# Kernel optimization log

Measured on AMD Instinct MI355X. Metric: run time of the kernel, lower is better.

## Reference

```python
import jax, jax.numpy as jnp
import numpy as np

N_ATOMS = 50000
N_NBRS = 32
R_CUTOFF = 5.0
N_BASIS = 128
N_FILTERS = 128
N_GAUSS = 25
MAX_Z = 100
MEAN = 0.0
STDDEV = 20.0


def ssp(x):
    # shifted softplus: softplus(x) - log(2)
    return jax.nn.softplus(x) - jnp.log(2.0)


def setup_inputs() -> dict:
    key = jax.random.key(0)
    ks = jax.random.split(key, 18)
    dR = jax.random.uniform(ks[0], (N_ATOMS, N_NBRS), dtype=jnp.float32) * R_CUTOFF
    Z = jax.random.randint(ks[1], (N_ATOMS,), 0, MAX_Z)
    nbr_idx = jax.random.randint(ks[2], (N_ATOMS, N_NBRS), 0, N_ATOMS)

    def p(k, shape):
        fan_in = shape[0]
        return (jax.random.normal(k, shape, dtype=jnp.float32) / np.sqrt(fan_in)).astype(jnp.float32)

    return dict(
        dR=dR, Z=Z, nbr_idx=nbr_idx,
        embed_table=jax.random.normal(ks[3], (MAX_Z, N_BASIS), dtype=jnp.float32),
        fw1=p(ks[4], (N_GAUSS, N_FILTERS)), fb1=jnp.zeros((N_FILTERS,), jnp.float32),
        fw2=p(ks[5], (N_FILTERS, N_FILTERS)), fb2=jnp.zeros((N_FILTERS,), jnp.float32),
        in2f_w=p(ks[6], (N_BASIS, N_FILTERS)),
        f2out_w1=p(ks[7], (N_FILTERS, N_BASIS)), f2out_b1=jnp.zeros((N_BASIS,), jnp.float32),
        f2out_w2=p(ks[8], (N_BASIS, N_BASIS)), f2out_b2=jnp.zeros((N_BASIS,), jnp.float32),
        mlp_w1=p(ks[9], (N_BASIS, 64)), mlp_b1=jnp.zeros((64,), jnp.float32),
        mlp_w2=p(ks[10], (64, 1)), mlp_b2=jnp.zeros((1,), jnp.float32),
    )


def reference(dR, Z, nbr_idx, embed_table, fw1, fb1, fw2, fb2, in2f_w,
              f2out_w1, f2out_b1, f2out_w2, f2out_b2,
              mlp_w1, mlp_b1, mlp_w2, mlp_b2):
    # embedding lookup: [N, B]
    x = embed_table[Z]

    # gaussian smearing of distances: [N, K, G]
    offsets = jnp.linspace(0.0, R_CUTOFF, N_GAUSS, dtype=jnp.float32)
    coeff = -0.5 / (offsets[1] - offsets[0]) ** 2
    dr_exp = jnp.exp(coeff * (dR[..., None] - offsets) ** 2)

    # filter network: Dense+ssp, Dense -> [N, K, F]
    W = ssp(jnp.einsum('nkg,gf->nkf', dr_exp, fw1) + fb1)
    W = jnp.einsum('nkf,fh->nkh', W, fw2) + fb2

    # cosine cutoff
    fcut = 0.5 * (jnp.cos(dR * jnp.pi / R_CUTOFF) + 1.0) * (dR < R_CUTOFF)
    W = W * fcut[..., None]

    # cfconv: in2f (no bias), neighbor gather, elementwise filter, sum over neighbors
    y = x @ in2f_w                    # [N, F]
    y_nbrs = y[nbr_idx]               # [N, K, F] irregular gather
    mask = (nbr_idx < N_ATOMS)[..., None]
    agg = jnp.sum(jnp.where(mask, y_nbrs * W, 0.0), axis=1)  # [N, F]

    # f2out: Dense+ssp, Dense
    v = ssp(agg @ f2out_w1 + f2out_b1) @ f2out_w2 + f2out_b2

    # residual update
    x = x + v

    # atomwise MLP [128 -> 64 -> 1] with ssp between layers
    yi = ssp(x @ mlp_w1 + mlp_b1) @ mlp_w2 + mlp_b2  # [N, 1]
    yi = yi * STDDEV + MEAN

    # aggregate (sum over atom axis), per_atom=False
    return jnp.sum(yi, axis=0)  # [1]
```

## Files before the change

### kernel.cpp

```cpp
#include <hip/hip_runtime.h>
#include <math.h>

#define N_ATOMS  50000
#define N_NBRS   32
#define N_GAUSS  25
#define RCUT     5.0f
#define TT       192
#define TROWS    32
#define NTB      6
#define MAXZ     100
#define NT32     1563
#define PBLOCKS  256
#define NPAIR    (N_ATOMS * N_NBRS)
#define PKPAD    (NT32 * 1024)
#define PKB      782
#define PI_F     3.14159265358979323846f

typedef unsigned int   uint_t;
typedef unsigned short ushort_t;
typedef _Float16 f16;
typedef f16   f16x2 __attribute__((ext_vector_type(2)));
typedef f16   f16x4 __attribute__((ext_vector_type(4)));
typedef f16   f16x8 __attribute__((ext_vector_type(8)));
typedef float f32x4 __attribute__((ext_vector_type(4)));

__device__ __forceinline__ float ssp(float x) {
  return fmaxf(x, 0.0f) + __logf(fmaf(0.5f, __expf(-fabsf(x)), 0.5f));
}
__device__ __forceinline__ f16x2 bch(uint_t u) {
  return __builtin_bit_cast(f16x2, u);
}
__device__ __forceinline__ uint_t hcb(f16x2 v) {
  return __builtin_bit_cast(uint_t, v);
}
__device__ __forceinline__ int swz(int m, int e) {
  return m * 128 + ((((e >> 3) ^ m) & 15) << 3) + (e & 7);
}

__global__ void __launch_bounds__(256, 2)
prep_all_kernel(const float* __restrict__ fw1,
                const float* __restrict__ fb1,
                const float* __restrict__ fw2,
                const float* __restrict__ fb2,
                const float* __restrict__ w1,
                const float* __restrict__ w2,
                const float* __restrict__ mw1,
                const float* __restrict__ embed,
                const float* __restrict__ in2f,
                const float* __restrict__ dR,
                const int* __restrict__ nbr,
                const int* __restrict__ Z,
                f16* __restrict__ tabh,
                f16* __restrict__ ytab,
                f16* __restrict__ w1ht,
                f16* __restrict__ w2ht,
                f16* __restrict__ mw1ht,
                uint_t* __restrict__ pkAll) {
  const int tid = threadIdx.x;
  const int bid = blockIdx.x;

  __shared__ float sW2[128 * 128];
  __shared__ float sH[TROWS][128];

  if (bid >= NTB + 64) {
    const int base = (bid - NTB - 64) * 2048;
    #pragma unroll
    for (int t0 = 0; t0 < 8; ++t0) {
      const int idx = base + t0 * 256 + tid;
      if (idx < PKPAD) {
        uint_t pk = 0;
        if (idx < NPAIR) {
          const float r = dR[idx];
          const int  nb = nbr[idx];
          int i0 = (int)(r * (191.0f / RCUT) + 0.5f);
          i0 = min(i0, 191);
          pk = (uint_t)i0 | ((uint_t)Z[nb] << 8);
        }
        pkAll[idx] = pk;
      }
    }
    return;
  }

  if (bid < NTB) {
    const int i0 = bid * TROWS;
    #pragma unroll
    for (int t = 0; t < 16; ++t) {
      const int e = tid + t * 256;
      ((float4*)sW2)[e] = ((const float4*)fw2)[e];
    }
    {
      const int f  = tid & 127;
      const int rh = (tid >> 7) * (TROWS / 2);
      const float delta = RCUT / (float)(N_GAUSS - 1);
      const float coeff = -0.5f / (delta * delta);
      const float b1v = fb1[f];
      for (int j = 0; j < TROWS / 2; ++j) {
        const float r = (float)(i0 + rh + j) * (RCUT / 191.0f);
        float h = b1v;
        #pragma unroll
        for (int g = 0; g < N_GAUSS; ++g) {
          const float d = r - (float)g * delta;
          h = fmaf(__expf(coeff * d * d), fw1[g * 128 + f], h);
        }
        sH[rh + j][f] = ssp(h);
      }
    }
    __syncthreads();
    {
      const int c0 = (tid & 31) * 4;
      const int rg = (tid >> 5) * 4;
      f32x4 acc[4];
      const float4 bv = *(const float4*)&fb2[c0];
      #pragma unroll
      for (int j = 0; j < 4; ++j) acc[j] = (f32x4){bv.x, bv.y, bv.z, bv.w};
      for (int k = 0; k < 128; ++k) {
        const float4 wv = *(const float4*)&sW2[k * 128 + c0];
        #pragma unroll
        for (int j = 0; j < 4; ++j) {
          const float hv = sH[rg + j][k];
          acc[j][0] = fmaf(hv, wv.x, acc[j][0]);
          acc[j][1] = fmaf(hv, wv.y, acc[j][1]);
          acc[j][2] = fmaf(hv, wv.z, acc[j][2]);
          acc[j][3] = fmaf(hv, wv.w, acc[j][3]);
        }
      }
      #pragma unroll
      for (int j = 0; j < 4; ++j) {
        const int i = i0 + rg + j;
        const float r = (float)i * (RCUT / 191.0f);
        const float fc = (r < RCUT) ? 0.5f * (__cosf(r * PI_F / RCUT) + 1.0f) : 0.0f;
        f16x4 o;
        #pragma unroll
        for (int c = 0; c < 4; ++c) o[c] = (f16)(acc[j][c] * fc);
        *(f16x4*)&tabh[i * 128 + c0] = o;
      }
    }
  } else {
    const int cc = (bid - NTB) * 2 + (tid >> 7);
    const int i  = tid & 127;
    w1ht[cc * 128 + i] = (f16)w1[i * 128 + cc];
    w2ht[cc * 128 + i] = (f16)w2[i * 128 + cc];
    if (cc < 64) mw1ht[cc * 128 + i] = (f16)mw1[i * 64 + cc];
    float* xs = &sH[0][0] + (tid >> 7) * 128;
    xs[i] = (cc < MAXZ) ? embed[cc * 128 + i] : 0.0f;
    __syncthreads();
    if (cc < MAXZ) {
      float acc = 0.0f;
      for (int j = 0; j < 128; j += 4) {
        const float4 xv = *reinterpret_cast<const float4*>(&xs[j]);
        acc = fmaf(xv.x, in2f[(j + 0) * 128 + i], acc);
        acc = fmaf(xv.y, in2f[(j + 1) * 128 + i], acc);
        acc = fmaf(xv.z, in2f[(j + 2) * 128 + i], acc);
        acc = fmaf(xv.w, in2f[(j + 3) * 128 + i], acc);
      }
      ytab[cc * 128 + i] = (f16)acc;
    }
  }
}

__global__ void __launch_bounds__(512, 2)
fused_kernel(const uint_t* __restrict__ pkAll,
             const int* __restrict__ Z,
             const float* __restrict__ embed,
             const f16* __restrict__ tabh,
             const f16* __restrict__ ytab,
             const f16* __restrict__ w1ht, const float* __restrict__ b1,
             const f16* __restrict__ w2ht, const float* __restrict__ b2,
             const f16* __restrict__ mw1ht, const float* __restrict__ mb1,
             const float* __restrict__ mw2,
             float* __restrict__ partial) {
  const int tid = threadIdx.x;
  const int w   = tid >> 6;
  const int l   = tid & 63;
  const int q   = l >> 4;
  const int cq  = l & 15;
  const int bid = blockIdx.x;

  __shared__ __align__(16) f16    sW[TT * 128];
  __shared__ __align__(16) f16    sYT[MAXZ * 128];
  __shared__ __align__(16) uint_t s_pk[2][1024];
  __shared__ __align__(16) f16    aggB[2][32 * 128];
  __shared__ __align__(16) f16    sB[32 * 128];
  __shared__ __align__(16) f16    sX[32 * 128];
  __shared__ int   sZb[2][32];
  __shared__ float sRed[8];

  for (int e = tid; e < TT * 16; e += 512)   ((uint4*)sW)[e]  = ((const uint4*)tabh)[e];
  for (int e = tid; e < MAXZ * 16; e += 512) ((uint4*)sYT)[e] = ((const uint4*)ytab)[e];

  const int g   = w >> 2;
  const int wvg = w & 3;
  const int rc  = cq;
  const int qk  = q;
  f16x8 bw1[2][4], bw2[2][4], bwm[4];
  float bb1[2], bb2[2];
  #pragma unroll
  for (int t = 0; t < 2; ++t) {
    const int c = wvg * 32 + t * 16 + rc;
    bb1[t] = b1[c];
    bb2[t] = b2[c];
    #pragma unroll
    for (int k0i = 0; k0i < 4; ++k0i) {
      bw1[t][k0i] = *(const f16x8*)&w1ht[c * 128 + k0i * 32 + qk * 8];
      bw2[t][k0i] = *(const f16x8*)&w2ht[c * 128 + k0i * 32 + qk * 8];
    }
  }
  const int c1 = wvg * 16 + rc;
  #pragma unroll
  for (int k0i = 0; k0i < 4; ++k0i)
    bwm[k0i] = *(const f16x8*)&mw1ht[c1 * 128 + k0i * 32 + qk * 8];
  const float bm = mb1[c1];
  const float cm = mw2[c1];

  const int m = w * 4 + q;
  const char* wb = (const char*)sW  + cq * 16;
  const char* yb = (const char*)sYT + cq * 16;

  const int myChunks = (NT32 - 1 - bid) / PBLOCKS + 1;
  float vsum = 0.0f;

  f16x2 acc[4];
  uint4 twA[4], ytA[4], twB[4], ytB[4];

#define STAGE(bb, cc) { \
    const uint2 v = *(const uint2*)&pkAll[(cc) * 1024 + tid * 2]; \
    *(uint2*)&s_pk[bb][tid * 2] = v; \
    if (tid < 32) sZb[bb][tid] = ((cc) * 32 + tid < N_ATOMS) ? Z[(cc) * 32 + tid] : 0; }

#define IG(BK, bb, gi) { \
    _Pragma("unroll") \
    for (int d = 0; d < 4; ++d) { \
      const uint_t pk = s_pk[bb][m * N_NBRS + (gi) * 4 + d]; \
      tw##BK[d] = *(const uint4*)(wb + ((pk & 0xFFu) << 8)); \
      yt##BK[d] = *(const uint4*)(yb + ((pk >> 8) << 8)); \
    } }

#define CG(BK) { \
    _Pragma("unroll") \
    for (int d = 0; d < 4; ++d) { \
      acc[0] += bch(tw##BK[d].x) * bch(yt##BK[d].x); \
      acc[1] += bch(tw##BK[d].y) * bch(yt##BK[d].y); \
      acc[2] += bch(tw##BK[d].z) * bch(yt##BK[d].z); \
      acc[3] += bch(tw##BK[d].w) * bch(yt##BK[d].w); \
    } }

#define AGGW(bb) { \
    uint4 o; \
    o.x = hcb(acc[0]); o.y = hcb(acc[1]); o.z = hcb(acc[2]); o.w = hcb(acc[3]); \
    const int mm = m & 15; \
    *(uint4*)&aggB[bb][(m >> 4) * 2048 + mm * 128 + (((cq ^ mm) & 15) << 3)] = o; }

#define AFRAGP(P, k0) (*(const f16x8*)&(P)[rc * 128 + (((((k0) >> 3) + qk) ^ rc) & 15) * 8])

  STAGE(0, bid)
  if (1 < myChunks) STAGE(1, bid + PBLOCKS)
  __syncthreads();
  #pragma unroll
  for (int c = 0; c < 4; ++c) acc[c] = (f16x2)0;
  IG(A, 0, 0) IG(B, 0, 1)
  CG(A) IG(A, 0, 2)
  CG(B) IG(B, 0, 3)
  CG(A) IG(A, 0, 4)
  CG(B) IG(B, 0, 5)
  CG(A) IG(A, 0, 6)
  CG(B) IG(B, 0, 7)
  CG(A)
  CG(B)
  AGGW(0)
  __syncthreads();

  for (int s = 0; s < myChunks; ++s) {
    const int b  = s & 1;
    const int cc = bid + s * PBLOCKS;
    const bool hn = (s + 1 < myChunks);
    const int nb_ = b ^ 1;

    if (hn) {
      #pragma unroll
      for (int c = 0; c < 4; ++c) acc[c] = (f16x2)0;
    }

    if (hn) { IG(A, nb_, 0) IG(B, nb_, 1) }
    {
      const f16* aggp = &aggB[b][g * 2048];
      f32x4 dacc[2];
      #pragma unroll
      for (int t = 0; t < 2; ++t) dacc[t] = (f32x4){bb1[t], bb1[t], bb1[t], bb1[t]};
      #pragma unroll
      for (int k0i = 0; k0i < 4; ++k0i) {
        const f16x8 af = AFRAGP(aggp, k0i * 32);
        #pragma unroll
        for (int t = 0; t < 2; ++t)
          dacc[t] = __builtin_amdgcn_mfma_f32_16x16x32_f16(af, bw1[t][k0i], dacc[t], 0, 0, 0);
      }
      f16* hB = &sB[g * 2048];
      #pragma unroll
      for (int t = 0; t < 2; ++t) {
        const int c = wvg * 32 + t * 16 + rc;
        #pragma unroll
        for (int r = 0; r < 4; ++r) hB[swz(qk * 4 + r, c)] = (f16)ssp(dacc[t][r]);
      }
    }
    if (hn) { CG(A) IG(A, nb_, 2) CG(B) CG(A) }
    __syncthreads();

    if (hn) { IG(A, nb_, 3) IG(B, nb_, 4) }
    {
      const f16* hB = &sB[g * 2048];
      f16* hX = &sX[g * 2048];
      f32x4 dacc[2];
      #pragma unroll
      for (int t = 0; t < 2; ++t) dacc[t] = (f32x4){bb2[t], bb2[t], bb2[t], bb2[t]};
      #pragma unroll
      for (int k0i = 0; k0i < 4; ++k0i) {
        const f16x8 af = AFRAGP(hB, k0i * 32);
        #pragma unroll
        for (int t = 0; t < 2; ++t)
          dacc[t] = __builtin_amdgcn_mfma_f32_16x16x32_f16(af, bw2[t][k0i], dacc[t], 0, 0, 0);
      }
      #pragma unroll
      for (int t = 0; t < 2; ++t) {
        const int c = wvg * 32 + t * 16 + rc;
        #pragma unroll
        for (int r = 0; r < 4; ++r) {
          const int mm = qk * 4 + r;
          const float x = embed[(size_t)sZb[b][g * 16 + mm] * 128 + c] + dacc[t][r];
          hX[swz(mm, c)] = (f16)x;
        }
      }
    }
    if (hn) { CG(A) IG(A, nb_, 5) CG(B) CG(A) }
    __syncthreads();

    if (hn) { IG(A, nb_, 6) IG(B, nb_, 7) }
    if (s + 2 < myChunks) STAGE(b, bid + (s + 2) * PBLOCKS)
    {
      const f16* hX = &sX[g * 2048];
      f32x4 a2 = (f32x4){bm, bm, bm, bm};
      #pragma unroll
      for (int k0i = 0; k0i < 4; ++k0i)
        a2 = __builtin_amdgcn_mfma_f32_16x16x32_f16(AFRAGP(hX, k0i * 32), bwm[k0i], a2, 0, 0, 0);
      #pragma unroll
      for (int r = 0; r < 4; ++r) {
        const int atom = cc * 32 + g * 16 + qk * 4 + r;
        if (atom < N_ATOMS) vsum = fmaf(ssp(a2[r]), cm, vsum);
      }
    }
    if (hn) { CG(A) CG(B) AGGW(nb_) }
    __syncthreads();
  }
#undef STAGE
#undef IG
#undef CG
#undef AGGW
#undef AFRAGP

  #pragma unroll
  for (int o = 1; o < 64; o <<= 1) vsum += __shfl_xor(vsum, o, 64);
  if (l == 0) sRed[w] = vsum;
  __syncthreads();
  if (tid == 0) {
    float sF = 0.0f;
    #pragma unroll
    for (int i = 0; i < 8; ++i) sF += sRed[i];
    partial[bid] = sF;
  }
}

__global__ void __launch_bounds__(256, 1)
reduce_kernel(const float* __restrict__ partial,
              const float* __restrict__ mb2,
              float* __restrict__ out) {
  const int tid = threadIdx.x;
  float s = 0.0f;
  for (int i = tid; i < PBLOCKS; i += 256) s += partial[i];
  __shared__ float sr[4];
  #pragma unroll
  for (int o = 1; o < 64; o <<= 1) s += __shfl_xor(s, o, 64);
  if ((tid & 63) == 0) sr[tid >> 6] = s;
  __syncthreads();
  if (tid == 0) {
    out[0] = 20.0f * (sr[0] + sr[1] + sr[2] + sr[3] + (float)N_ATOMS * mb2[0]);
  }
}

extern "C" void kernel_launch(void* const* d_in, const int* in_sizes, int n_in,
                              void* d_out, int out_size, void* d_ws, size_t ws_size,
                              hipStream_t stream) {
  const float* dR    = (const float*)d_in[0];
  const int*   Z     = (const int*)  d_in[1];
  const int*   nbr   = (const int*)  d_in[2];
  const float* embed = (const float*)d_in[3];
  const float* fw1   = (const float*)d_in[4];
  const float* fb1   = (const float*)d_in[5];
  const float* fw2   = (const float*)d_in[6];
  const float* fb2   = (const float*)d_in[7];
  const float* in2f  = (const float*)d_in[8];
  const float* w1    = (const float*)d_in[9];
  const float* b1    = (const float*)d_in[10];
  const float* w2    = (const float*)d_in[11];
  const float* b2    = (const float*)d_in[12];
  const float* mw1   = (const float*)d_in[13];
  const float* mb1   = (const float*)d_in[14];
  const float* mw2   = (const float*)d_in[15];
  const float* mb2   = (const float*)d_in[16];
  float* out = (float*)d_out;

  char* ws = (char*)d_ws;
  f16*    tabh    = (f16*)ws;
  f16*    ytab    = (f16*)(ws + (size_t)64 * 1024);
  f16*    w1ht    = (f16*)(ws + (size_t)128 * 1024);
  f16*    w2ht    = (f16*)(ws + (size_t)192 * 1024);
  f16*    mw1ht   = (f16*)(ws + (size_t)256 * 1024);
  float*  partial = (float*)(ws + (size_t)384 * 1024);
  uint_t* pkAll   = (uint_t*)(ws + (size_t)1024 * 1024);

  prep_all_kernel<<<NTB + 64 + PKB, 256, 0, stream>>>(fw1, fb1, fw2, fb2,
      w1, w2, mw1, embed, in2f, dR, nbr, Z,
      tabh, ytab, w1ht, w2ht, mw1ht, pkAll);
  fused_kernel<<<PBLOCKS, 512, 0, stream>>>(pkAll, Z, embed,
      tabh, ytab, w1ht, b1, w2ht, b2, mw1ht, mb1, mw2, partial);
  reduce_kernel<<<1, 256, 0, stream>>>(partial, mb2, out);
}
```

Baseline: 53.38 us.

## Process 64 atoms per chunk with two atoms per gather thread

Each pipeline iteration now covers 64 atoms instead of 32. Every thread accumulates neighbor sums for two atoms, and every wave runs the dense MFMA stages on two 16-row tiles. The goal is to halve the number of block barriers and pipeline iterations per atom and to give the gather more independent work to overlap with the MFMA stages. In exchange, LDS use grows to roughly 150KB. Chunk granularity is also coarser across the 256 blocks, so the most loaded block may now handle more atoms than before.

```diff
diff --git a/kernel.cpp b/kernel.cpp
--- a/kernel.cpp
+++ b/kernel.cpp
@@ -9,10 +9,10 @@
 #define TROWS    32
 #define NTB      6
 #define MAXZ     100
-#define NT32     1563
+#define NT64     782
 #define PBLOCKS  256
 #define NPAIR    (N_ATOMS * N_NBRS)
-#define PKPAD    (NT32 * 1024)
+#define PKPAD    (NT64 * 2048)
 #define PKB      782
 #define PI_F     3.14159265358979323846f
 
@@ -179,17 +179,17 @@
 
   __shared__ __align__(16) f16    sW[TT * 128];
   __shared__ __align__(16) f16    sYT[MAXZ * 128];
-  __shared__ __align__(16) uint_t s_pk[2][1024];
-  __shared__ __align__(16) f16    aggB[2][32 * 128];
-  __shared__ __align__(16) f16    sB[32 * 128];
-  __shared__ __align__(16) f16    sX[32 * 128];
-  __shared__ int   sZb[2][32];
+  __shared__ __align__(16) uint_t s_pk[2][2048];
+  __shared__ __align__(16) f16    aggB[2][64 * 128];
+  __shared__ __align__(16) f16    sB[64 * 128];
+  __shared__ __align__(16) f16    sX[64 * 128];
+  __shared__ int   sZb[2][64];
   __shared__ float sRed[8];
 
   for (int e = tid; e < TT * 16; e += 512)   ((uint4*)sW)[e]  = ((const uint4*)tabh)[e];
   for (int e = tid; e < MAXZ * 16; e += 512) ((uint4*)sYT)[e] = ((const uint4*)ytab)[e];
 
-  const int g   = w >> 2;
+  const int gg  = w >> 2;
   const int wvg = w & 3;
   const int rc  = cq;
   const int qk  = q;
@@ -213,60 +213,81 @@
   const float bm = mb1[c1];
   const float cm = mw2[c1];
 
-  const int m = w * 4 + q;
+  const int m0q = w * 8 + q * 2;
   const char* wb = (const char*)sW  + cq * 16;
   const char* yb = (const char*)sYT + cq * 16;
 
-  const int myChunks = (NT32 - 1 - bid) / PBLOCKS + 1;
+  const int myChunks = (NT64 - 1 - bid) / PBLOCKS + 1;
   float vsum = 0.0f;
 
-  f16x2 acc[4];
+  f16x2 acc[2][4];
   uint4 twA[4], ytA[4], twB[4], ytB[4];
 
 #define STAGE(bb, cc) { \
-    const uint2 v = *(const uint2*)&pkAll[(cc) * 1024 + tid * 2]; \
-    *(uint2*)&s_pk[bb][tid * 2] = v; \
-    if (tid < 32) sZb[bb][tid] = ((cc) * 32 + tid < N_ATOMS) ? Z[(cc) * 32 + tid] : 0; }
+    const uint4 v = *(const uint4*)&pkAll[(size_t)(cc) * 2048 + tid * 4]; \
+    *(uint4*)&s_pk[bb][tid * 4] = v; \
+    if (tid < 64) sZb[bb][tid] = ((cc) * 64 + tid < N_ATOMS) ? Z[(cc) * 64 + tid] : 0; }
 
 #define IG(BK, bb, gi) { \
     _Pragma("unroll") \
     for (int d = 0; d < 4; ++d) { \
-      const uint_t pk = s_pk[bb][m * N_NBRS + (gi) * 4 + d]; \
+      const int s = (gi) * 4 + d; \
+      const uint_t pk = s_pk[bb][(m0q + (s >> 5)) * N_NBRS + (s & 31)]; \
       tw##BK[d] = *(const uint4*)(wb + ((pk & 0xFFu) << 8)); \
       yt##BK[d] = *(const uint4*)(yb + ((pk >> 8) << 8)); \
     } }
 
-#define CG(BK) { \
+#define CG(BK, gi) { \
     _Pragma("unroll") \
     for (int d = 0; d < 4; ++d) { \
-      acc[0] += bch(tw##BK[d].x) * bch(yt##BK[d].x); \
-      acc[1] += bch(tw##BK[d].y) * bch(yt##BK[d].y); \
-      acc[2] += bch(tw##BK[d].z) * bch(yt##BK[d].z); \
-      acc[3] += bch(tw##BK[d].w) * bch(yt##BK[d].w); \
+      const int al = (((gi) * 4 + d) >> 5); \
+      acc[al][0] += bch(tw##BK[d].x) * bch(yt##BK[d].x); \
+      acc[al][1] += bch(tw##BK[d].y) * bch(yt##BK[d].y); \
+      acc[al][2] += bch(tw##BK[d].z) * bch(yt##BK[d].z); \
+      acc[al][3] += bch(tw##BK[d].w) * bch(yt##BK[d].w); \
     } }
 
 #define AGGW(bb) { \
-    uint4 o; \
-    o.x = hcb(acc[0]); o.y = hcb(acc[1]); o.z = hcb(acc[2]); o.w = hcb(acc[3]); \
-    const int mm = m & 15; \
-    *(uint4*)&aggB[bb][(m >> 4) * 2048 + mm * 128 + (((cq ^ mm) & 15) << 3)] = o; }
+    _Pragma("unroll") \
+    for (int al = 0; al < 2; ++al) { \
+      uint4 o; \
+      o.x = hcb(acc[al][0]); o.y = hcb(acc[al][1]); \
+      o.z = hcb(acc[al][2]); o.w = hcb(acc[al][3]); \
+      const int am = m0q + al; \
+      const int mm = am & 15; \
+      *(uint4*)&aggB[bb][(am >> 4) * 2048 + mm * 128 + (((cq ^ mm) & 15) << 3)] = o; \
+    } }
+
+#define ACCZ { \
+    _Pragma("unroll") \
+    for (int al = 0; al < 2; ++al) { \
+      _Pragma("unroll") \
+      for (int c = 0; c < 4; ++c) acc[al][c] = (f16x2)0; \
+    } }
 
 #define AFRAGP(P, k0) (*(const f16x8*)&(P)[rc * 128 + (((((k0) >> 3) + qk) ^ rc) & 15) * 8])
 
   STAGE(0, bid)
   if (1 < myChunks) STAGE(1, bid + PBLOCKS)
   __syncthreads();
-  #pragma unroll
-  for (int c = 0; c < 4; ++c) acc[c] = (f16x2)0;
+  ACCZ
   IG(A, 0, 0) IG(B, 0, 1)
-  CG(A) IG(A, 0, 2)
-  CG(B) IG(B, 0, 3)
-  CG(A) IG(A, 0, 4)
-  CG(B) IG(B, 0, 5)
-  CG(A) IG(A, 0, 6)
-  CG(B) IG(B, 0, 7)
-  CG(A)
-  CG(B)
+  CG(A, 0) IG(A, 0, 2)
+  CG(B, 1) IG(B, 0, 3)
+  CG(A, 2) IG(A, 0, 4)
+  CG(B, 3) IG(B, 0, 5)
+  CG(A, 4) IG(A, 0, 6)
+  CG(B, 5) IG(B, 0, 7)
+  CG(A, 6) IG(A, 0, 8)
+  CG(B, 7) IG(B, 0, 9)
+  CG(A, 8) IG(A, 0, 10)
+  CG(B, 9) IG(B, 0, 11)
+  CG(A, 10) IG(A, 0, 12)
+  CG(B, 11) IG(B, 0, 13)
+  CG(A, 12) IG(A, 0, 14)
+  CG(B, 13) IG(B, 0, 15)
+  CG(A, 14)
+  CG(B, 15)
   AGGW(0)
   __syncthreads();
 
@@ -276,14 +297,14 @@
     const bool hn = (s + 1 < myChunks);
     const int nb_ = b ^ 1;
 
-    if (hn) {
-      #pragma unroll
-      for (int c = 0; c < 4; ++c) acc[c] = (f16x2)0;
-    }
+    if (hn) ACCZ
 
     if (hn) { IG(A, nb_, 0) IG(B, nb_, 1) }
-    {
-      const f16* aggp = &aggB[b][g * 2048];
+    #pragma unroll
+    for (int ti = 0; ti < 2; ++ti) {
+      const int tt = gg * 2 + ti;
+      const f16* aggp = &aggB[b][tt * 2048];
+      f16* hB = &sB[tt * 2048];
       f32x4 dacc[2];
       #pragma unroll
       for (int t = 0; t < 2; ++t) dacc[t] = (f32x4){bb1[t], bb1[t], bb1[t], bb1[t]};
@@ -294,7 +315,6 @@
         for (int t = 0; t < 2; ++t)
           dacc[t] = __builtin_amdgcn_mfma_f32_16x16x32_f16(af, bw1[t][k0i], dacc[t], 0, 0, 0);
       }
-      f16* hB = &sB[g * 2048];
       #pragma unroll
       for (int t = 0; t < 2; ++t) {
         const int c = wvg * 32 + t * 16 + rc;
@@ -302,13 +322,21 @@
         for (int r = 0; r < 4; ++r) hB[swz(qk * 4 + r, c)] = (f16)ssp(dacc[t][r]);
       }
     }
-    if (hn) { CG(A) IG(A, nb_, 2) CG(B) CG(A) }
+    if (hn) {
+      CG(A, 0) IG(A, nb_, 2)
+      CG(B, 1) IG(B, nb_, 3)
+      CG(A, 2) IG(A, nb_, 4)
+      CG(B, 3)
+      CG(A, 4)
+    }
     __syncthreads();
 
-    if (hn) { IG(A, nb_, 3) IG(B, nb_, 4) }
-    {
-      const f16* hB = &sB[g * 2048];
-      f16* hX = &sX[g * 2048];
+    if (hn) { IG(A, nb_, 5) IG(B, nb_, 6) }
+    #pragma unroll
+    for (int ti = 0; ti < 2; ++ti) {
+      const int tt = gg * 2 + ti;
+      const f16* hB = &sB[tt * 2048];
+      f16* hX = &sX[tt * 2048];
       f32x4 dacc[2];
       #pragma unroll
       for (int t = 0; t < 2; ++t) dacc[t] = (f32x4){bb2[t], bb2[t], bb2[t], bb2[t]};
@@ -325,35 +353,52 @@
         #pragma unroll
         for (int r = 0; r < 4; ++r) {
           const int mm = qk * 4 + r;
-          const float x = embed[(size_t)sZb[b][g * 16 + mm] * 128 + c] + dacc[t][r];
+          const float x = embed[(size_t)sZb[b][tt * 16 + mm] * 128 + c] + dacc[t][r];
           hX[swz(mm, c)] = (f16)x;
         }
       }
     }
-    if (hn) { CG(A) IG(A, nb_, 5) CG(B) CG(A) }
+    if (hn) {
+      CG(A, 5) IG(A, nb_, 7)
+      CG(B, 6) IG(B, nb_, 8)
+      CG(A, 7) IG(A, nb_, 9)
+      CG(B, 8)
+      CG(A, 9)
+    }
     __syncthreads();
 
-    if (hn) { IG(A, nb_, 6) IG(B, nb_, 7) }
+    if (hn) { IG(A, nb_, 10) IG(B, nb_, 11) }
     if (s + 2 < myChunks) STAGE(b, bid + (s + 2) * PBLOCKS)
-    {
-      const f16* hX = &sX[g * 2048];
+    #pragma unroll
+    for (int ti = 0; ti < 2; ++ti) {
+      const int tt = gg * 2 + ti;
+      const f16* hX = &sX[tt * 2048];
       f32x4 a2 = (f32x4){bm, bm, bm, bm};
       #pragma unroll
       for (int k0i = 0; k0i < 4; ++k0i)
         a2 = __builtin_amdgcn_mfma_f32_16x16x32_f16(AFRAGP(hX, k0i * 32), bwm[k0i], a2, 0, 0, 0);
       #pragma unroll
       for (int r = 0; r < 4; ++r) {
-        const int atom = cc * 32 + g * 16 + qk * 4 + r;
+        const int atom = cc * 64 + tt * 16 + qk * 4 + r;
         if (atom < N_ATOMS) vsum = fmaf(ssp(a2[r]), cm, vsum);
       }
     }
-    if (hn) { CG(A) CG(B) AGGW(nb_) }
+    if (hn) {
+      CG(A, 10) IG(A, nb_, 12)
+      CG(B, 11) IG(B, nb_, 13)
+      CG(A, 12) IG(A, nb_, 14)
+      CG(B, 13) IG(B, nb_, 15)
+      CG(A, 14)
+      CG(B, 15)
+      AGGW(nb_)
+    }
     __syncthreads();
   }
 #undef STAGE
 #undef IG
 #undef CG
 #undef AGGW
+#undef ACCZ
 #undef AFRAGP
 
   #pragma unroll
```

After: 57.72 us. +8.1%, slower.
